# Performance work log

Hardware: AMD Instinct MI355X
Metric: run time of the kernel (lower is better)

The kernel has to match this reference:

```python
import jax, jax.numpy as jnp
import numpy as np

PI = np.pi
B_IN, B1, B2 = 30, 10, 6      # bandwidths: input S2, after conv1, after conv2
F1, F2, F_OUT = 20, 40, 10


def _wigner_d_stack(l, betas):
    """Wigner-d d^l_{mn}(beta) = <m|exp(-i beta Jy)|n> (real), shape [nbeta, 2l+1, 2l+1]."""
    n = 2 * l + 1
    m = np.arange(-l, l)
    c = np.sqrt(l * (l + 1) - m * (m + 1))          # J+ couplings m -> m+1
    Jp = np.zeros((n, n))
    Jp[np.arange(1, n), np.arange(n - 1)] = c
    A = 0.5 * (Jp.T - Jp)                            # exp(beta*A) = d^l(beta)
    ev, V = np.linalg.eig(A)
    Vi = np.linalg.inv(V)
    E = np.exp(np.multiply.outer(np.asarray(betas, np.float64), ev))
    return np.einsum('mk,bk,kn->bmn', V, E, Vi).real


def _qw(b):
    """Driscoll-Healy quadrature weights over beta for the SOFT grid of bandwidth b."""
    j = np.arange(2 * b)
    theta = PI * (2 * j + 1) / (4 * b)
    k = np.arange(b)
    return (2.0 / b) * np.sin(theta) * (np.sin(theta[:, None] * (2 * k + 1)) / (2 * k + 1)).sum(1)


def _betas(b):
    return PI * (2 * np.arange(2 * b) + 1) / (4 * b)


def _s2_grid():   # s2_near_identity_grid(): 3 betas x 8 alphas = 24 points
    beta = np.arange(1, 4) * (PI / 8) / 3
    alpha = np.linspace(0, 2 * PI, 8, endpoint=False)
    B, A = np.meshgrid(beta, alpha, indexing='ij')
    return B.ravel(), A.ravel()


def _so3_grid():  # so3_near_identity_grid(): 3x8x8 = 192 points, gamma = pre_gamma - alpha
    beta = np.arange(1, 4) * (PI / 8) / 3
    alpha = np.linspace(0, 2 * PI, 8, endpoint=False)
    pre_gamma = np.linspace(-2 * PI, 2 * PI, 8, endpoint=False)
    B, A, C = np.meshgrid(beta, alpha, pre_gamma, indexing='ij')
    return B.ravel(), A.ravel(), (C - A).ravel()


# ---------- static spectral constants (numpy, built once at import) ----------
_bet_in, _w_in = _betas(B_IN), _qw(B_IN)
_bet1, _w1 = _betas(B1), _qw(B1)
_bet2, _w2 = _betas(B2), _qw(B2)
_gb, _ga = _s2_grid()
_gb3, _ga3, _gc3 = _so3_grid()

# conv1 analysis: w(beta) * d^l_{m0}(beta_in), flattened over (l,m), l < B1
_dm1, _mi1, _y1 = [], [], []
for l in range(B1):
    d = _wigner_d_stack(l, _bet_in)                        # [60, 2l+1, 2l+1]
    _dm1.append((d[:, :, l] * _w_in[:, None]).T)           # [2l+1, 60] (column n=0)
    m = np.arange(-l, l + 1)
    _mi1.append(m % (2 * B_IN))
    dg = _wigner_d_stack(l, _gb)[:, :, l]                  # [24, 2l+1]
    _y1.append(np.exp(-1j * np.outer(m, _ga)) * dg.T)      # kernel rft basis [2l+1, 24]
DM1 = np.concatenate(_dm1, 0).astype(np.float32)           # [100, 60]
MI1 = np.concatenate(_mi1, 0)
Y1B = np.concatenate(_y1, 0).astype(np.complex64)          # [100, 24]

D_B1 = [_wigner_d_stack(l, _bet1) for l in range(B1)]      # d^l at the 20 betas of b=10 grid

# conv2 analysis: w(beta) * d^l_{mn}(beta_1), flattened over (l,m,n), l < B2
_dm2, _mi2, _ni2, _y2 = [], [], [], []
for l in range(B2):
    m = np.arange(-l, l + 1)
    d = D_B1[l]                                            # [20, 2l+1, 2l+1]
    _dm2.append((d * _w1[:, None, None]).reshape(2 * B1, -1).T)   # [(2l+1)^2, 20]
    mm, nn = np.meshgrid(m, m, indexing='ij')
    _mi2.append(mm.ravel() % (2 * B1))
    _ni2.append(nn.ravel() % (2 * B1))
    dg = _wigner_d_stack(l, _gb3)                          # [192, 2l+1, 2l+1]
    ph = np.exp(-1j * (np.multiply.outer(m, _ga3)[:, None, :] +
                       np.multiply.outer(m, _gc3)[None, :, :]))   # [2l+1,2l+1,192]
    _y2.append((np.moveaxis(dg, 0, -1) * ph).reshape(-1, _gb3.size))
DM2 = np.concatenate(_dm2, 0).astype(np.float32)           # [286, 20]
MI2 = np.concatenate(_mi2, 0)
NI2 = np.concatenate(_ni2, 0)
Y2B = np.concatenate(_y2, 0).astype(np.complex64)          # [286, 192]

D_B1F = [d.astype(np.float32) for d in D_B1]
D_B2F = [_wigner_d_stack(l, _bet2).astype(np.float32) for l in range(B2)]

SC1 = np.float32(1.0 / np.sqrt(_gb.size * 1))    # kernel scalings (s2cnn-style init scale)
SC2 = np.float32(1.0 / np.sqrt(_gb3.size * F1))
W2J = _w2.astype(np.float32)
INTEG_SCALE = np.float32((2 * PI / (2 * B2)) ** 2)


def _forward(x, kernel1, kernel2, w_out, bias_out):
    Bt = x.shape[0]
    # ---- S2Convolution: S2-FFT(x), rft(kernel), s2_mm, SO3-iFFT ----
    xh = jnp.fft.fft(x, axis=-1) / (2 * B_IN)                     # [B,1,60,60] cplx (alpha FFT)
    xg = xh[..., jnp.asarray(MI1)]                                # [B,1,60,100]
    X = jnp.einsum('kj,bfjk->kbf', jnp.asarray(DM1), xg)          # [100,B,1] spectral F^l_m
    Yk = jnp.einsum('kg,iog->kio', jnp.asarray(Y1B), kernel1.astype(jnp.complex64)) * SC1
    S = jnp.zeros((Bt, F1, 2 * B1, 2 * B1, 2 * B1), jnp.complex64)
    off = 0
    for l in range(B1):
        L = 2 * l + 1
        Z = jnp.einsum('mbi,nio->mnbo', X[off:off + L], jnp.conj(Yk[off:off + L]))
        T = jnp.einsum('jmn,mnbo->bojmn', float(2 * l + 1) * jnp.asarray(D_B1F[l]), Z)
        mi = np.arange(-l, l + 1) % (2 * B1)
        S = S.at[:, :, :, mi[:, None], mi[None, :]].add(T)
        off += L
    x1 = jnp.fft.ifft2(S, axes=(-2, -1)).real * float((2 * B1) ** 2)   # [B,F1,20,20,20]
    x1 = jax.nn.relu(x1)
    # ---- SO3Convolution: SO3-FFT, rft(kernel), so3_mm, SO3-iFFT ----
    xh2 = jnp.fft.fft2(x1, axes=(-2, -1)) / float((2 * B1) ** 2)       # alpha,gamma FFT
    xg2 = xh2[:, :, :, jnp.asarray(MI2), jnp.asarray(NI2)]             # [B,F1,20,286]
    X2 = jnp.einsum('kj,bfjk->kbf', jnp.asarray(DM2), xg2)             # [286,B,F1]
    Yk2 = jnp.einsum('kg,iog->kio', jnp.asarray(Y2B), kernel2.astype(jnp.complex64)) * SC2
    S2 = jnp.zeros((Bt, F2, 2 * B2, 2 * B2, 2 * B2), jnp.complex64)
    off = 0
    for l in range(B2):
        L = 2 * l + 1
        X2l = X2[off:off + L * L].reshape(L, L, Bt, F1)     # [m,k,B,i]
        Y2l = Yk2[off:off + L * L].reshape(L, L, F1, F2)    # [n,k,i,o]
        Z = jnp.einsum('mkbi,nkio->mnbo', X2l, jnp.conj(Y2l))   # hat z^l = hat x^l hat y^l+
        T = jnp.einsum('jmn,mnbo->bojmn', float(2 * l + 1) * jnp.asarray(D_B2F[l]), Z)
        mi = np.arange(-l, l + 1) % (2 * B2)
        S2 = S2.at[:, :, :, mi[:, None], mi[None, :]].add(T)
        off += L * L
    x2 = jnp.fft.ifft2(S2, axes=(-2, -1)).real * float((2 * B2) ** 2)  # [B,F2,12,12,12]
    x2 = jax.nn.relu(x2)
    # ---- so3_integrate + linear head ----
    feat = INTEG_SCALE * jnp.einsum('bfjac,j->bf', x2, jnp.asarray(W2J))
    return feat @ w_out.T + bias_out


def setup_inputs() -> dict:
    key = jax.random.key(0)
    ks = jax.random.split(key, 5)
    return {
        'x': jax.random.normal(ks[0], (128, 1, 2 * B_IN, 2 * B_IN), jnp.float32),
        'kernel1': jax.random.normal(ks[1], (1, F1, 24), jnp.float32),
        'kernel2': jax.random.normal(ks[2], (F1, F2, 192), jnp.float32),
        'w_out': jax.random.normal(ks[3], (F_OUT, F2), jnp.float32) / np.sqrt(float(F2)),
        'bias_out': jax.random.normal(ks[4], (F_OUT,), jnp.float32) * 0.01,
    }


def reference(x, kernel1, kernel2, w_out, bias_out):
    return _forward(x, kernel1, kernel2, w_out, bias_out)
```

## Files before the change

kernel.cpp:

```cpp
#include <hip/hip_runtime.h>
#include <cmath>

#define NT 256
#define BT 128

#define OFF_W60   0
#define OFF_E20   2280
#define OFF_E12   2320
#define OFF_W2J   2344
#define OFF_DM1   2356
#define OFF_Y1B   8356
#define OFF_D1R   13156
#define OFF_DM2   39756
#define OFF_Y2B   45476
#define OFF_D2R   155300
#define OFF_T19U  158732
#define OFF_T11V  159492
#define OFF_T12U  159932
#define OFF_TABA  160196
#define OFF_TABB  161526
#define OFF_TH19  161812
#define OFF_TH12  162212
#define OFF_TABH  162356
#define OFF_TAH1  162504
#define OFF_DM2T  163220
#define OFF_TGIX  168940
#define OFF_QW30  169228
#define OFF_QW10  169288
#define OFF_QW6   169308
#define OFF_D3B   169320
#define OFF_PA    170178
#define OFF_PG    170354
#define OFF_END   171764
#define N_INIT1   1742
#define N_INIT2   109735

__constant__ int c_ZB1[10] = {0,1,10,35,84,165,286,455,680,969};
__constant__ int c_ZBH[10] = {0,1,7,22,50,95,161,252,372,525};
__constant__ int c_ZB2[6]  = {0,1,10,35,84,165};
__constant__ int c_BOFF[6] = {0,22,208,718,1712,3350};

__device__ inline void wsync() {
    __asm__ volatile("" ::: "memory");
    __builtin_amdgcn_s_waitcnt(0xC07F);
    __builtin_amdgcn_wave_barrier();
    __asm__ volatile("" ::: "memory");
}

__device__ inline double dipow(double x, int e) {
    double r = 1.0;
    for (int i = 0; i < e; ++i) r *= x;
    return r;
}

__device__ double wigd(const double* F, const double* Fi, int l, int mp, int m, double beta) {
    double cb = cos(beta * 0.5), sb = sin(beta * 0.5);
    int smin = m - mp; if (smin < 0) smin = 0;
    int smax = l + m;  if (l - mp < smax) smax = l - mp;
    double pref = sqrt(F[l+mp] * F[l-mp] * F[l+m] * F[l-m]);
    double sum = 0.0;
    for (int s = smin; s <= smax; ++s) {
        double t = pref * (Fi[l+m-s] * Fi[s] * Fi[mp-m+s] * Fi[l-mp-s]);
        t *= dipow(cb, 2*l + m - mp - 2*s) * dipow(sb, mp - m + 2*s);
        sum += ((mp - m + s) & 1) ? -t : t;
    }
    return sum;
}

__device__ double qwj(int bnd, int j) {
    const double PI = 3.14159265358979323846;
    double theta = PI * (2*j + 1) / (4.0 * bnd);
    double s = 0.0;
    for (int k = 0; k < bnd; ++k) s += sin(theta * (2*k + 1)) / (2*k + 1);
    return 2.0 / bnd * sin(theta) * s;
}

__global__ void k_init1(float* __restrict__ ws) {
    int idx = blockIdx.x * blockDim.x + threadIdx.x;
    if (idx >= N_INIT1) return;
    double F[20], Fi[20];
    F[0] = 1.0;
    #pragma unroll
    for (int i = 1; i < 20; ++i) F[i] = F[i-1] * i;
    Fi[19] = 1.0 / F[19];
    #pragma unroll
    for (int i = 18; i >= 0; --i) Fi[i] = Fi[i+1] * (i+1);
    const double PI = 3.14159265358979323846;

    if (idx < 60) {
        ws[OFF_QW30 + idx] = (float)qwj(30, idx);
    } else if (idx < 80) {
        ws[OFF_QW10 + idx - 60] = (float)qwj(10, idx - 60);
    } else if (idx < 92) {
        ws[OFF_QW6 + idx - 80] = (float)qwj(6, idx - 80);
    } else if (idx < 950) {
        int e = idx - 92; int k2 = e / 3, bi = e % 3;
        int l = 0; while (l < 5 && k2 >= c_ZB2[l+1]) ++l;
        int L = 2*l + 1, loc = k2 - c_ZB2[l];
        int m = loc / L - l, n = loc % L - l;
        double beta = (bi + 1) * (PI / 8.0) / 3.0;
        ws[OFF_D3B + e] = (float)wigd(F, Fi, l, m, n, beta);
    } else if (idx < 1038) {
        int e = idx - 950; int m = e / 8 - 5, ai = e % 8;
        double ph = -(double)m * (2.0 * PI * ai / 8.0);
        ws[OFF_PA + 2*e]     = (float)cos(ph);
        ws[OFF_PA + 2*e + 1] = (float)sin(ph);
    } else {
        int e = idx - 1038; int n = e / 64 - 5, g2 = e % 64, ai = g2 / 8, ci = g2 % 8;
        double alpha = 2.0 * PI * ai / 8.0;
        double gamma = (-2.0 * PI + ci * (PI / 2.0)) - alpha;
        double ph = -(double)n * gamma;
        ws[OFF_PG + 2*e]     = (float)cos(ph);
        ws[OFF_PG + 2*e + 1] = (float)sin(ph);
    }
}

__global__ void k_init2(float* __restrict__ ws) {
    int idx = blockIdx.x * blockDim.x + threadIdx.x;
    if (idx >= N_INIT2) return;
    double F[20], Fi[20];
    F[0] = 1.0;
    #pragma unroll
    for (int i = 1; i < 20; ++i) F[i] = F[i-1] * i;
    Fi[19] = 1.0 / F[19];
    #pragma unroll
    for (int i = 18; i >= 0; --i) Fi[i] = Fi[i+1] * (i+1);
    const double PI = 3.14159265358979323846;

    if (idx < 1140) {
        int r = idx / 60, a = idx % 60;
        double ang = -2.0 * PI * (double)((r - 9) * a) / 60.0;
        ws[OFF_W60 + 2*idx]     = (float)cos(ang);
        ws[OFF_W60 + 2*idx + 1] = (float)sin(ang);
    } else if (idx < 1160) {
        int t = idx - 1140;
        double ang = 2.0 * PI * t / 20.0;
        ws[OFF_E20 + 2*t]     = (float)cos(ang);
        ws[OFF_E20 + 2*t + 1] = (float)sin(ang);
    } else if (idx < 1172) {
        int t = idx - 1160;
        double ang = 2.0 * PI * t / 12.0;
        ws[OFF_E12 + 2*t]     = (float)cos(ang);
        ws[OFF_E12 + 2*t + 1] = (float)sin(ang);
    } else if (idx < 1184) {
        int j = idx - 1172;
        ws[OFF_W2J + j] = ws[OFF_QW6 + j];
    } else if (idx < 7184) {
        int e = idx - 1184; int k = e / 60, j = e % 60;
        int l = 0; while ((l + 1) * (l + 1) <= k) ++l;
        int m = k - l*l - l;
        double beta = PI * (2*j + 1) / 120.0;
        ws[OFF_DM1 + e] = (float)((double)ws[OFF_QW30 + j] * wigd(F, Fi, l, m, 0, beta));
    } else if (idx < 9584) {
        int e = idx - 7184; int k = e / 24, g = e % 24;
        int l = 0; while ((l + 1) * (l + 1) <= k) ++l;
        int m = k - l*l - l;
        int bi = g / 8, ai = g % 8;
        double beta  = (bi + 1) * (PI / 8.0) / 3.0;
        double alpha = 2.0 * PI * ai / 8.0;
        double d = wigd(F, Fi, l, m, 0, beta);
        double ph = -(double)m * alpha;
        ws[OFF_Y1B + 2*e]     = (float)(d * cos(ph));
        ws[OFF_Y1B + 2*e + 1] = (float)(d * sin(ph));
    } else if (idx < 36184) {
        int e = idx - 9584; int j = e / 1330, t = e % 1330;
        int l = 0; while (l < 9 && t >= c_ZB1[l+1]) ++l;
        int L = 2*l + 1, loc = t - c_ZB1[l];
        int mi = loc / L, ni = loc % L;
        double beta = PI * (2*j + 1) / 40.0;
        ws[OFF_D1R + e] = (float)((double)L * wigd(F, Fi, l, mi - l, ni - l, beta));
    } else if (idx < 41904) {
    } else if (idx < 96816) {
        int e = idx - 41904; int k2 = e / 192, g = e % 192;
        int l = 0; while (l < 5 && k2 >= c_ZB2[l+1]) ++l;
        int L = 2*l + 1, loc = k2 - c_ZB2[l];
        int m = loc / L - l, n = loc % L - l;
        int bi = g / 64, ai = (g / 8) % 8, ci = g % 8;
        float d = ws[OFF_D3B + k2 * 3 + bi];
        const float2 pa = ((const float2*)(ws + OFF_PA))[(m + 5) * 8 + ai];
        const float2 pg = ((const float2*)(ws + OFF_PG))[(n + 5) * 64 + ai * 8 + ci];
        ws[OFF_Y2B + 2*e]     = d * (pa.x * pg.x - pa.y * pg.y);
        ws[OFF_Y2B + 2*e + 1] = d * (pa.x * pg.y + pa.y * pg.x);
    } else if (idx < 100248) {
        int e = idx - 96816; int j = e / 286, t = e % 286;
        int l = 0; while (l < 5 && t >= c_ZB2[l+1]) ++l;
        int L = 2*l + 1, loc = t - c_ZB2[l];
        int mi = loc / L, ni = loc % L;
        double beta = PI * (2*j + 1) / 24.0;
        ws[OFF_D2R + e] = (float)((double)L * wigd(F, Fi, l, mi - l, ni - l, beta));
    } else if (idx < 100628) {
        int e = idx - 100248; int c = e / 19, n = e % 19 - 9;
        double ang = 2.0 * PI * (double)(n * c) / 20.0;
        ws[OFF_T19U + 2*e]     = (float)cos(ang);
        ws[OFF_T19U + 2*e + 1] = (float)sin(ang);
    } else if (idx < 100848) {
        int e = idx - 100628; int r = e / 20, c = e % 20;
        double ang = -2.0 * PI * (double)((r - 5) * c) / 20.0;
        ws[OFF_T11V + 2*e]     = (float)cos(ang);
        ws[OFF_T11V + 2*e + 1] = (float)sin(ang);
    } else if (idx < 100980) {
        int e = idx - 100848; int c = e / 11, n = e % 11 - 5;
        double ang = 2.0 * PI * (double)(n * c) / 12.0;
        ws[OFF_T12U + 2*e]     = (float)cos(ang);
        ws[OFF_T12U + 2*e + 1] = (float)sin(ang);
    } else if (idx < 102310) {
    } else if (idx < 102596) {
        int t = idx - 102310;
        int l = 0; while (l < 5 && t >= c_ZB2[l+1]) ++l;
        int L = 2*l + 1, loc = t - c_ZB2[l];
        ((int*)ws)[OFF_TABB + t] = l | ((loc / L) << 8) | ((loc % L) << 16);
    } else if (idx < 102796) {
        int e = idx - 102596; int a = e / 10, mm = e % 10;
        double f = (mm == 0) ? 1.0 : 2.0;
        double ang = 2.0 * PI * (double)(mm * a) / 20.0;
        ws[OFF_TH19 + 2*e]     = (float)(f * cos(ang));
        ws[OFF_TH19 + 2*e + 1] = (float)(f * sin(ang));
    } else if (idx < 102868) {
        int e = idx - 102796; int a = e / 6, mm = e % 6;
        double f = (mm == 0) ? 1.0 : 2.0;
        double ang = 2.0 * PI * (double)(mm * a) / 12.0;
        ws[OFF_TH12 + 2*e]     = (float)(f * cos(ang));
        ws[OFF_TH12 + 2*e + 1] = (float)(f * sin(ang));
    } else if (idx < 103014) {
        int t = idx - 102868;
        int l = 0, cum = 0, loc = 0;
        for (; l < 6; ++l) {
            int L = 2*l + 1, h = (L*L + 1) / 2;
            if (t < cum + h) { loc = t - cum; break; }
            cum += h;
        }
        ((int*)ws)[OFF_TABH + t] = l | (loc << 8);
    } else if (idx < 103729) {
        int t = idx - 103014;
        int l = 0; while (l < 9 && t >= c_ZBH[l+1]) ++l;
        int L = 2*l + 1, loc = t - c_ZBH[l];
        ((int*)ws)[OFF_TAH1 + t] = l | ((loc / L) << 8) | ((loc % L) << 16);
    } else if (idx < 109449) {
        int e = idx - 103729; int k2 = e / 20, j = e % 20;
        int l = 0; while (l < 5 && k2 >= c_ZB2[l+1]) ++l;
        int L = 2*l + 1, loc = k2 - c_ZB2[l];
        int mi = loc / L, ni = loc % L;
        double beta = PI * (2*j + 1) / 40.0;
        ws[OFF_DM2T + e] = (float)((double)ws[OFF_QW10 + j] *
                                   wigd(F, Fi, l, mi - l, ni - l, beta) / 400.0);
    } else {
        int t = idx - 109449;
        int l = 0; while (l < 5 && t >= c_ZB2[l+1]) ++l;
        int L = 2*l + 1, loc = t - c_ZB2[l];
        int m = loc / L - l, n = loc % L - l;
        int gi, sgbit;
        if (m >= 0) { gi = m * 11 + (n + 5); sgbit = 0; }
        else        { gi = (-m) * 11 + (5 - n); sgbit = 1; }
        ((int*)ws)[OFF_TGIX + t] = gi | (sgbit << 16);
    }
}

__global__ void k_dft_alpha(const float* __restrict__ x, const float2* __restrict__ W60,
                            float2* __restrict__ xh) {
    int idx = blockIdx.x * blockDim.x + threadIdx.x;
    if (idx >= BT * 60 * 19) return;
    int r = idx % 19;
    int j = (idx / 19) % 60;
    int b = idx / (19 * 60);
    const float* xr = x + (b * 60 + j) * 60;
    const float2* wr = W60 + r * 60;
    float re = 0.f, im = 0.f;
    for (int a = 0; a < 60; ++a) {
        float v = xr[a];
        float2 w = wr[a];
        re += v * w.x; im += v * w.y;
    }
    xh[idx] = make_float2(re * (1.f / 60.f), im * (1.f / 60.f));
}

__global__ void k_X1Y1(const float2* __restrict__ xh, const float* __restrict__ DM1,
                       float2* __restrict__ X, const float* __restrict__ k1,
                       const float2* __restrict__ Y1B, float2* __restrict__ Yk1) {
    int bid = blockIdx.x;
    if (bid < 50) {
        int idx = bid * NT + threadIdx.x;
        if (idx >= 100 * BT) return;
        int b = idx % BT, k = idx / BT;
        int l = 0; while ((l + 1) * (l + 1) <= k) ++l;
        int r = (k - l*l - l) + 9;
        float re = 0.f, im = 0.f;
        for (int j = 0; j < 60; ++j) {
            float d = DM1[k * 60 + j];
            float2 v = xh[(b * 60 + j) * 19 + r];
            re += d * v.x; im += d * v.y;
        }
        X[k * BT + b] = make_float2(re, im);
    } else {
        int idx = (bid - 50) * NT + threadIdx.x;
        if (idx >= 100 * 20) return;
        int o = idx % 20, k = idx / 20;
        float re = 0.f, im = 0.f;
        for (int g = 0; g < 24; ++g) {
            float2 y = Y1B[k * 24 + g];
            float w = k1[o * 24 + g];
            re += y.x * w; im += y.y * w;
        }
        const float SC1 = 0.20412414523193154f;
        Yk1[idx] = make_float2(re * SC1, im * SC1);
    }
}

__global__ __launch_bounds__(NT) void k_Yk2(const float* __restrict__ k2in,
                                            const float2* __restrict__ Y2B,
                                            const int* __restrict__ gTABH,
                                            float2* __restrict__ Yk2) {
    const int h = blockIdx.x >> 1;
    const int half = blockIdx.x & 1;
    const int tid = threadIdx.x;
    int ph = gTABH[h];
    int l = ph & 255, loc = ph >> 8;
    int L = 2 * l + 1;
    int mi = loc / L, ni = loc % L;
    int k2  = c_ZB2[l] + loc;
    int locm = L * L - 1 - loc;
    int k2m = c_ZB2[l] + locm;
    float par = ((mi + ni) & 1) ? -1.f : 1.f;

    __shared__ __align__(16) float2 sY[192];
    for (int t = tid; t < 192; t += NT) sY[t] = Y2B[k2 * 192 + t];
    __syncthreads();
    const float4* sY4 = (const float4*)sY;
    const float SC2 = 0.016137430609197573f;
    for (int t = half * 400 + tid; t < half * 400 + 400; t += NT) {
        int o = t / 20, i = t % 20;
        const float4* kp = (const float4*)(k2in + (i * 40 + o) * 192);
        float re = 0.f, im = 0.f;
        #pragma unroll 4
        for (int p = 0; p < 48; ++p) {
            float4 w = kp[p];
            float4 y01 = sY4[2*p], y23 = sY4[2*p + 1];
            re += w.x * y01.x + w.y * y01.z + w.z * y23.x + w.w * y23.z;
            im += w.x * y01.y + w.y * y01.w + w.z * y23.y + w.w * y23.w;
        }
        re *= SC2; im *= SC2;
        Yk2[(o * 286 + k2) * 20 + i] = make_float2(re, im);
        if (k2m != k2)
            Yk2[(o * 286 + k2m) * 20 + i] = make_float2(par * re, -par * im);
    }
}

__global__ __launch_bounds__(NT) void k_stage1(
    const float2* __restrict__ X, const float2* __restrict__ Yk1,
    const float* __restrict__ gD1R,
    const float2* __restrict__ gT19, const float2* __restrict__ gT11,
    const float2* __restrict__ gTH19,
    const int* __restrict__ gTAH1, float2* __restrict__ Gg) {
    const int b = blockIdx.x % BT;
    const int f = blockIdx.x / BT;
    const int tid = threadIdx.x;
    const int wv = tid >> 6, lane = tid & 63;

    __shared__ __align__(16) float2 sZ[715];
    __shared__ __align__(16) float2 sT19[440];
    __shared__ __align__(16) float2 sTH19[280];
    __shared__ __align__(16) float2 sT11[220];
    __shared__ __align__(16) float2 sA[4][224];
    __shared__ __align__(16) float2 sB[4][280];

    for (int t = tid; t < 380; t += NT) sT19[(t / 19) * 22 + (t % 19)] = gT19[t];
    for (int t = tid; t < 200; t += NT) sTH19[(t / 10) * 14 + (t % 10)] = gTH19[t];
    for (int t = tid; t < 220; t += NT) sT11[t] = gT11[t];
    for (int t = tid; t < 715; t += NT) {
        int p = gTAH1[t];
        int l = p & 255, mm = (p >> 8) & 255, ni = p >> 16;
        float2 a = X[(l*l + l + mm) * BT + b];
        float2 y = Yk1[(l*l + ni) * 20 + f];
        sZ[t] = make_float2(a.x * y.x + a.y * y.y, a.y * y.x - a.x * y.y);
    }
    __syncthreads();

    float2* S   = sA[wv];
    float2* U   = sB[wv];
    float*  x1  = (float*)sA[wv];
    float2* V   = sB[wv];

    for (int jj = 0; jj < 5; ++jj) {
        const int j = wv + 4 * jj;

        {
            const float* dp = gD1R + j * 1330;
            for (int t = lane; t < 190; t += 64) {
                int mm = t / 19, ni = t % 19;
                int n = ni - 9;
                int an = n < 0 ? -n : n;
                int lmin = mm > an ? mm : an;
                float re = 0.f, im = 0.f;
                for (int l = lmin; l < 10; ++l) {
                    int L = 2*l + 1;
                    float dv = dp[c_ZB1[l] + (mm + l) * L + (n + l)];
                    float2 z = sZ[c_ZBH[l] + mm * L + (n + l)];
                    re += dv * z.x; im += dv * z.y;
                }
                S[mm * 22 + ni] = make_float2(re, im);
            }
        }
        wsync();

        for (int t = lane; t < 100; t += 64) {
            int mm = t / 10, c = t % 10;
            const float4* sp = (const float4*)(S + mm * 22);
            const float4* tp = (const float4*)(sT19 + c * 22);
            float re_e = 0.f, im_e = 0.f, re_o = 0.f, im_o = 0.f;
            #pragma unroll
            for (int p = 0; p < 9; ++p) {
                float4 s = sp[p], w = tp[p];
                re_o += s.x * w.x - s.y * w.y;  im_o += s.x * w.y + s.y * w.x;
                re_e += s.z * w.z - s.w * w.w;  im_e += s.z * w.w + s.w * w.z;
            }
            {
                float2 s1 = S[mm * 22 + 18], w1 = sT19[c * 22 + 18];
                re_o += s1.x * w1.x - s1.y * w1.y;
                im_o += s1.x * w1.y + s1.y * w1.x;
            }
            U[c * 14 + mm]        = make_float2(re_e + re_o, im_e + im_o);
            U[(c + 10) * 14 + mm] = make_float2(re_e - re_o, im_e - im_o);
        }
        wsync();

        for (int t = lane; t < 100; t += 64) {
            int cp = t % 10, ap = t / 10;
            const float4* u0 = (const float4*)(U + cp * 14);
            const float4* u1 = (const float4*)(U + (cp + 10) * 14);
            const float4* tp = (const float4*)(sTH19 + ap * 14);
            float e0 = 0.f, o0 = 0.f, e1 = 0.f, o1 = 0.f;
            #pragma unroll
            for (int p = 0; p < 5; ++p) {
                float4 w = tp[p];
                float4 ua = u0[p], ub = u1[p];
                e0 += ua.x * w.x - ua.y * w.y;
                o0 += ua.z * w.z - ua.w * w.w;
                e1 += ub.x * w.x - ub.y * w.y;
                o1 += ub.z * w.z - ub.w * w.w;
            }
            float v;
            v = e0 + o0; x1[ap * 20 + cp]             = v > 0.f ? v : 0.f;
            v = e0 - o0; x1[(ap + 10) * 20 + cp]      = v > 0.f ? v : 0.f;
            v = e1 + o1; x1[ap * 20 + cp + 10]        = v > 0.f ? v : 0.f;
            v = e1 - o1; x1[(ap + 10) * 20 + cp + 10] = v > 0.f ? v : 0.f;
        }
        wsync();

        for (int t = lane; t < 120; t += 64) {
            int nn = t / 20, a = t % 20;
            const float4* xp = (const float4*)(x1 + a * 20);
            const float4* tp = (const float4*)(sT11 + (nn + 5) * 20);
            float r0 = 0.f, i0 = 0.f, r1 = 0.f, i1 = 0.f;
            #pragma unroll
            for (int p = 0; p < 5; ++p) {
                float4 xv = xp[p];
                float4 t01 = tp[2*p], t23 = tp[2*p + 1];
                r0 += xv.x * t01.x + xv.y * t01.z;
                i0 += xv.x * t01.y + xv.y * t01.w;
                r1 += xv.z * t23.x + xv.w * t23.z;
                i1 += xv.z * t23.y + xv.w * t23.w;
            }
            V[nn * 22 + a] = make_float2(r0 + r1, i0 + i1);
        }
        wsync();

        for (int t = lane; t < 66; t += 64) {
            int mm = t / 11, ni2 = t % 11;
            int nn2 = ni2 - 5;
            int na = nn2 < 0 ? -nn2 : nn2;
            float s = nn2 < 0 ? -1.f : 1.f;
            const float4* vp = (const float4*)(V + na * 22);
            const float4* tp = (const float4*)(sT11 + (mm + 5) * 20);
            float r0 = 0.f, i0 = 0.f, r1 = 0.f, i1 = 0.f;
            #pragma unroll
            for (int q = 0; q < 10; ++q) {
                float4 v = vp[q], w = tp[q];
                float vy0 = s * v.y, vy1 = s * v.w;
                r0 += v.x * w.x - vy0 * w.y;
                i0 += v.x * w.y + vy0 * w.x;
                r1 += v.z * w.z - vy1 * w.w;
                i1 += v.z * w.w + vy1 * w.z;
            }
            Gg[((size_t)(b * 20 + f) * 20 + j) * 66 + t] = make_float2(r0 + r1, i0 + i1);
        }
        wsync();
    }
}

__global__ __launch_bounds__(NT) void k_X2c(
    const float2* __restrict__ Gg, const float* __restrict__ gDM2T,
    const int* __restrict__ gTGIX, float2* __restrict__ X2g) {
    const int b = blockIdx.x % BT;
    const int f = blockIdx.x / BT;
    const int tid = threadIdx.x;
    __shared__ __align__(16) float2 sG[1320];
    const float2* Gp = Gg + (size_t)(b * 20 + f) * 20 * 66;
    for (int t = tid; t < 1320; t += NT) sG[t] = Gp[t];
    __syncthreads();
    for (int k2 = tid; k2 < 286; k2 += NT) {
        int e = gTGIX[k2];
        int gi = e & 0xFFFF;
        float sg = (e >> 16) ? -1.f : 1.f;
        const float* dm = gDM2T + k2 * 20;
        float re = 0.f, im = 0.f;
        #pragma unroll
        for (int j = 0; j < 20; ++j) {
            float d = dm[j];
            float2 g = sG[j * 66 + gi];
            re += d * g.x; im += d * g.y;
        }
        X2g[b * 5720 + k2 * 20 + f] = make_float2(re, sg * im);
    }
}

__global__ __launch_bounds__(NT) void k_Z2(
    const float2* __restrict__ X2g, const float2* __restrict__ Yk2,
    const int* __restrict__ gTABB, const int* __restrict__ gTABH,
    float2* __restrict__ Z2g) {
    const int bt   = blockIdx.x & 15;
    const int part = (blockIdx.x >> 4) & 1;
    const int o    = blockIdx.x >> 5;
    const int b0 = bt * 8;
    const int tid = threadIdx.x;

    __shared__ __align__(16) float2 sB[3350];

    const int sub  = part ? 3350 : 0;
    const int stN  = part ? 2420 : 3300;
    const int k2b  = part ? 165 : 0;
    const float2* Bg = Yk2 + o * 5720 + k2b * 20;
    for (int e = tid; e < stN; e += NT) {
        int k2 = k2b + e / 20, i = e % 20;
        int p = gTABB[k2];
        int l = p & 255, r = (p >> 8) & 255, kk = p >> 16;
        sB[c_BOFF[l] - sub + r * (40 * l + 22) + kk * 20 + i] = Bg[e];
    }
    __syncthreads();

    const int perb  = part ? 61 : 85;
    const int hbase = part ? 85 : 0;
    for (int q = tid; q < 8 * perb; q += NT) {
        int b_local = q / perb, h = hbase + q % perb;
        int ph = gTABH[h];
        int l = ph & 255, loc = ph >> 8;
        int L = 2 * l + 1;
        int mi = loc / L, ni = loc % L;
        const float4* ap = (const float4*)(X2g + (size_t)(b0 + b_local) * 5720
                                           + (c_ZB2[l] + mi * L) * 20);
        const float4* bp = (const float4*)(sB + c_BOFF[l] - sub + ni * (40 * l + 22));
        float re = 0.f, im = 0.f;
        int n4 = 10 * L;
        for (int p4 = 0; p4 < n4; ++p4) {
            float4 a = ap[p4], y = bp[p4];
            re += a.x * y.x + a.y * y.y + a.z * y.z + a.w * y.w;
            im += a.y * y.x - a.x * y.y + a.w * y.z - a.z * y.w;
        }
        size_t base = ((size_t)(b0 + b_local) * 40 + o) * 286;
        Z2g[base + c_ZB2[l] + loc] = make_float2(re, im);
        int locm = L * L - 1 - loc;
        if (locm != loc) {
            float sg = ((mi + ni) & 1) ? -1.f : 1.f;
            Z2g[base + c_ZB2[l] + locm] = make_float2(sg * re, -sg * im);
        }
    }
}

__global__ __launch_bounds__(NT) void k_stage2b(
    const float2* __restrict__ Z2g, const float* __restrict__ gD2R,
    const float2* __restrict__ gT12, const float2* __restrict__ gTH12,
    const float* __restrict__ gW2J, float* __restrict__ feat) {
    const int b = blockIdx.x % BT;
    const int o = blockIdx.x / BT;
    const int tid = threadIdx.x;
    const int wv = tid >> 6, lane = tid & 63;

    __shared__ __align__(16) float2 sZb[286];
    __shared__ __align__(16) float2 sT12[168];
    __shared__ __align__(16) float2 sTH12[96];
    __shared__ __align__(16) float2 sS[4][88];
    __shared__ __align__(16) float2 sU[4][96];
    __shared__ float sredw[4];

    const float2* Zr = Z2g + ((size_t)b * 40 + o) * 286;
    for (int t = tid; t < 286; t += NT) sZb[t] = Zr[t];
    for (int t = tid; t < 132; t += NT) sT12[(t / 11) * 14 + (t % 11)] = gT12[t];
    for (int t = tid; t < 72; t += NT) sTH12[(t / 6) * 8 + (t % 6)] = gTH12[t];
    __syncthreads();

    float2* S = sS[wv];
    float2* U = sU[wv];
    float facc = 0.f;

    for (int jj = 0; jj < 3; ++jj) {
        const int j = wv + 4 * jj;

        {
            const float* dp = gD2R + j * 286;
            for (int t = lane; t < 66; t += 64) {
                int mm = t / 11, ni = t % 11;
                int n = ni - 5;
                int an = n < 0 ? -n : n;
                int lmin = mm > an ? mm : an;
                float re = 0.f, im = 0.f;
                for (int l = lmin; l < 6; ++l) {
                    int L = 2*l + 1;
                    int off = c_ZB2[l] + (mm + l) * L + (n + l);
                    float dv = dp[off];
                    float2 z = sZb[off];
                    re += dv * z.x; im += dv * z.y;
                }
                S[mm * 14 + ni] = make_float2(re, im);
            }
        }
        wsync();

        for (int t = lane; t < 72; t += 64) {
            int mm = t / 12, c = t % 12;
            const float4* sp = (const float4*)(S + mm * 14);
            const float4* tp = (const float4*)(sT12 + c * 14);
            float re = 0.f, im = 0.f;
            #pragma unroll
            for (int p = 0; p < 5; ++p) {
                float4 s = sp[p], w = tp[p];
                re += s.x * w.x - s.y * w.y + s.z * w.z - s.w * w.w;
                im += s.x * w.y + s.y * w.x + s.z * w.w + s.w * w.z;
            }
            float2 s1 = S[mm * 14 + 10], w1 = sT12[c * 14 + 10];
            re += s1.x * w1.x - s1.y * w1.y;
            im += s1.x * w1.y + s1.y * w1.x;
            U[c * 8 + mm] = make_float2(re, im);
        }
        wsync();

        {
            float wj = gW2J[j];
            for (int t = lane; t < 144; t += 64) {
                int a = t / 12, c = t % 12;
                const float4* up = (const float4*)(U + c * 8);
                const float4* tp = (const float4*)(sTH12 + a * 8);
                float acc = 0.f;
                #pragma unroll
                for (int p = 0; p < 3; ++p) {
                    float4 u = up[p], w = tp[p];
                    acc += u.x * w.x - u.y * w.y + u.z * w.z - u.w * w.w;
                }
                if (acc > 0.f) facc += wj * acc;
            }
        }
        wsync();
    }

    #pragma unroll
    for (int d = 32; d > 0; d >>= 1) facc += __shfl_down(facc, d, 64);
    if (lane == 0) sredw[wv] = facc;
    __syncthreads();
    if (tid == 0) {
        const float INTEG = 0.27415567780803774f;
        feat[b * 40 + o] = (sredw[0] + sredw[1] + sredw[2] + sredw[3]) * INTEG;
    }
}

__global__ void k_out(const float* __restrict__ feat, const float* __restrict__ w,
                      const float* __restrict__ bias, float* __restrict__ out) {
    int idx = blockIdx.x * blockDim.x + threadIdx.x;
    if (idx >= BT * 10) return;
    int fo = idx % 10, b = idx / 10;
    float acc = bias[fo];
    for (int o2 = 0; o2 < 40; ++o2) acc += feat[b * 40 + o2] * w[fo * 40 + o2];
    out[idx] = acc;
}

extern "C" void kernel_launch(void* const* d_in, const int* in_sizes, int n_in,
                              void* d_out, int out_size, void* d_ws, size_t ws_size,
                              hipStream_t stream) {
    (void)in_sizes; (void)n_in; (void)out_size; (void)ws_size;
    const float* x   = (const float*)d_in[0];
    const float* k1  = (const float*)d_in[1];
    const float* k2  = (const float*)d_in[2];
    const float* wO  = (const float*)d_in[3];
    const float* bO  = (const float*)d_in[4];
    float* out = (float*)d_out;

    float* ws = (float*)d_ws;
    const float2* cW60 = (const float2*)(ws + OFF_W60);
    const float*  cW2J = ws + OFF_W2J;
    const float*  cDM1 = ws + OFF_DM1;
    const float2* cY1B = (const float2*)(ws + OFF_Y1B);
    const float*  gD1R = ws + OFF_D1R;
    const float2* cY2B = (const float2*)(ws + OFF_Y2B);
    const float*  gD2R = ws + OFF_D2R;
    const float2* gT19 = (const float2*)(ws + OFF_T19U);
    const float2* gT11 = (const float2*)(ws + OFF_T11V);
    const float2* gT12 = (const float2*)(ws + OFF_T12U);
    const float2* gTH19 = (const float2*)(ws + OFF_TH19);
    const float2* gTH12 = (const float2*)(ws + OFF_TH12);
    const int*    gTABB = (const int*)(ws + OFF_TABB);
    const int*    gTABH = (const int*)(ws + OFF_TABH);
    const int*    gTAH1 = (const int*)(ws + OFF_TAH1);
    const float*  gDM2T = ws + OFF_DM2T;
    const int*    gTGIX = (const int*)(ws + OFF_TGIX);

    float2* xh   = (float2*)(ws + OFF_END);
    float2* X    = xh + BT * 60 * 19;
    float2* Yk1  = X + 100 * BT;
    float2* Yk2  = Yk1 + 100 * 20;
    float2* X2   = Yk2 + 40 * 286 * 20;
    float*  feat = (float*)(X2 + (size_t)BT * 5720);
    float2* Gg   = (float2*)(feat + BT * 40);
    float2* Z2   = Gg;

    k_init1<<<(N_INIT1 + NT - 1) / NT, NT, 0, stream>>>(ws);
    k_init2<<<(N_INIT2 + NT - 1) / NT, NT, 0, stream>>>(ws);
    k_dft_alpha<<<(BT * 60 * 19 + NT - 1) / NT, NT, 0, stream>>>(x, cW60, xh);
    k_X1Y1<<<58, NT, 0, stream>>>(xh, cDM1, X, k1, cY1B, Yk1);
    k_Yk2<<<292, NT, 0, stream>>>(k2, cY2B, gTABH, Yk2);
    k_stage1<<<BT * 20, NT, 0, stream>>>(X, Yk1, gD1R, gT19, gT11, gTH19, gTAH1, Gg);
    k_X2c<<<BT * 20, NT, 0, stream>>>(Gg, gDM2T, gTGIX, X2);
    k_Z2<<<1280, NT, 0, stream>>>(X2, Yk2, gTABB, gTABH, Z2);
    k_stage2b<<<BT * 40, NT, 0, stream>>>(Z2, gD2R, gT12, gTH12, cW2J, feat);
    k_out<<<(BT * 10 + NT - 1) / NT, NT, 0, stream>>>(feat, wO, bO, out);
}
```

Measured before the change: 397.5 us.

## Fuse alpha DFT with conv1 analysis and fold X2 contraction into stage1

```diff
diff --git a/kernel.cpp b/kernel.cpp
--- a/kernel.cpp
+++ b/kernel.cpp
@@ -255,43 +255,48 @@
     }
 }
 
-__global__ void k_dft_alpha(const float* __restrict__ x, const float2* __restrict__ W60,
-                            float2* __restrict__ xh) {
-    int idx = blockIdx.x * blockDim.x + threadIdx.x;
-    if (idx >= BT * 60 * 19) return;
-    int r = idx % 19;
-    int j = (idx / 19) % 60;
-    int b = idx / (19 * 60);
-    const float* xr = x + (b * 60 + j) * 60;
-    const float2* wr = W60 + r * 60;
-    float re = 0.f, im = 0.f;
-    for (int a = 0; a < 60; ++a) {
-        float v = xr[a];
-        float2 w = wr[a];
-        re += v * w.x; im += v * w.y;
-    }
-    xh[idx] = make_float2(re * (1.f / 60.f), im * (1.f / 60.f));
-}
-
-__global__ void k_X1Y1(const float2* __restrict__ xh, const float* __restrict__ DM1,
-                       float2* __restrict__ X, const float* __restrict__ k1,
-                       const float2* __restrict__ Y1B, float2* __restrict__ Yk1) {
-    int bid = blockIdx.x;
-    if (bid < 50) {
-        int idx = bid * NT + threadIdx.x;
-        if (idx >= 100 * BT) return;
-        int b = idx % BT, k = idx / BT;
-        int l = 0; while ((l + 1) * (l + 1) <= k) ++l;
-        int r = (k - l*l - l) + 9;
-        float re = 0.f, im = 0.f;
-        for (int j = 0; j < 60; ++j) {
-            float d = DM1[k * 60 + j];
-            float2 v = xh[(b * 60 + j) * 19 + r];
-            re += d * v.x; im += d * v.y;
-        }
-        X[k * BT + b] = make_float2(re, im);
+__global__ __launch_bounds__(NT) void k_front(
+    const float* __restrict__ x, const float2* __restrict__ W60,
+    const float* __restrict__ DM1, float2* __restrict__ X,
+    const float* __restrict__ k1, const float2* __restrict__ Y1B,
+    float2* __restrict__ Yk1) {
+    const int bid = blockIdx.x;
+    const int tid = threadIdx.x;
+    if (bid < BT) {
+        const int b = bid;
+        __shared__ __align__(16) float  sx[3600];
+        __shared__ __align__(16) float2 sW[1140];
+        __shared__ __align__(16) float2 sxh[1140];
+        for (int t = tid; t < 900; t += NT)
+            ((float4*)sx)[t] = ((const float4*)(x + b * 3600))[t];
+        for (int t = tid; t < 1140; t += NT) sW[t] = W60[t];
+        __syncthreads();
+        for (int t = tid; t < 1140; t += NT) {
+            int r = t % 19, j = t / 19;
+            const float* xr = sx + j * 60;
+            const float2* wr = sW + r * 60;
+            float re = 0.f, im = 0.f;
+            for (int a = 0; a < 60; ++a) {
+                float v = xr[a];
+                float2 w = wr[a];
+                re += v * w.x; im += v * w.y;
+            }
+            sxh[j * 19 + r] = make_float2(re * (1.f / 60.f), im * (1.f / 60.f));
+        }
+        __syncthreads();
+        for (int k = tid; k < 100; k += NT) {
+            int l = 0; while ((l + 1) * (l + 1) <= k) ++l;
+            int r = (k - l*l - l) + 9;
+            float re = 0.f, im = 0.f;
+            for (int j = 0; j < 60; ++j) {
+                float d = DM1[k * 60 + j];
+                float2 v = sxh[j * 19 + r];
+                re += d * v.x; im += d * v.y;
+            }
+            X[k * BT + b] = make_float2(re, im);
+        }
     } else {
-        int idx = (bid - 50) * NT + threadIdx.x;
+        int idx = (bid - BT) * NT + tid;
         if (idx >= 100 * 20) return;
         int o = idx % 20, k = idx / 20;
         float re = 0.f, im = 0.f;
@@ -349,7 +354,8 @@
     const float* __restrict__ gD1R,
     const float2* __restrict__ gT19, const float2* __restrict__ gT11,
     const float2* __restrict__ gTH19,
-    const int* __restrict__ gTAH1, float2* __restrict__ Gg) {
+    const int* __restrict__ gTAH1, const float* __restrict__ gDM2T,
+    const int* __restrict__ gTGIX, float2* __restrict__ X2g) {
     const int b = blockIdx.x % BT;
     const int f = blockIdx.x / BT;
     const int tid = threadIdx.x;
@@ -359,6 +365,7 @@
     __shared__ __align__(16) float2 sT19[440];
     __shared__ __align__(16) float2 sTH19[280];
     __shared__ __align__(16) float2 sT11[220];
+    __shared__ __align__(16) float2 sGall[1320];
     __shared__ __align__(16) float2 sA[4][224];
     __shared__ __align__(16) float2 sB[4][280];
 
@@ -480,22 +487,12 @@
                 r1 += v.z * w.z - vy1 * w.w;
                 i1 += v.z * w.w + vy1 * w.z;
             }
-            Gg[((size_t)(b * 20 + f) * 20 + j) * 66 + t] = make_float2(r0 + r1, i0 + i1);
+            sGall[j * 66 + t] = make_float2(r0 + r1, i0 + i1);
         }
         wsync();
     }
-}
-
-__global__ __launch_bounds__(NT) void k_X2c(
-    const float2* __restrict__ Gg, const float* __restrict__ gDM2T,
-    const int* __restrict__ gTGIX, float2* __restrict__ X2g) {
-    const int b = blockIdx.x % BT;
-    const int f = blockIdx.x / BT;
-    const int tid = threadIdx.x;
-    __shared__ __align__(16) float2 sG[1320];
-    const float2* Gp = Gg + (size_t)(b * 20 + f) * 20 * 66;
-    for (int t = tid; t < 1320; t += NT) sG[t] = Gp[t];
     __syncthreads();
+
     for (int k2 = tid; k2 < 286; k2 += NT) {
         int e = gTGIX[k2];
         int gi = e & 0xFFFF;
@@ -505,7 +502,7 @@
         #pragma unroll
         for (int j = 0; j < 20; ++j) {
             float d = dm[j];
-            float2 g = sG[j * 66 + gi];
+            float2 g = sGall[j * 66 + gi];
             re += d * g.x; im += d * g.y;
         }
         X2g[b * 5720 + k2 * 20 + f] = make_float2(re, sg * im);
@@ -564,7 +561,7 @@
     }
 }
 
-__global__ __launch_bounds__(NT) void k_stage2b(
+__global__ __launch_bounds__(128) void k_stage2b(
     const float2* __restrict__ Z2g, const float* __restrict__ gD2R,
     const float2* __restrict__ gT12, const float2* __restrict__ gTH12,
     const float* __restrict__ gW2J, float* __restrict__ feat) {
@@ -576,22 +573,22 @@
     __shared__ __align__(16) float2 sZb[286];
     __shared__ __align__(16) float2 sT12[168];
     __shared__ __align__(16) float2 sTH12[96];
-    __shared__ __align__(16) float2 sS[4][88];
-    __shared__ __align__(16) float2 sU[4][96];
-    __shared__ float sredw[4];
+    __shared__ __align__(16) float2 sS[2][88];
+    __shared__ __align__(16) float2 sU[2][96];
+    __shared__ float sredw[2];
 
     const float2* Zr = Z2g + ((size_t)b * 40 + o) * 286;
-    for (int t = tid; t < 286; t += NT) sZb[t] = Zr[t];
-    for (int t = tid; t < 132; t += NT) sT12[(t / 11) * 14 + (t % 11)] = gT12[t];
-    for (int t = tid; t < 72; t += NT) sTH12[(t / 6) * 8 + (t % 6)] = gTH12[t];
+    for (int t = tid; t < 286; t += 128) sZb[t] = Zr[t];
+    for (int t = tid; t < 132; t += 128) sT12[(t / 11) * 14 + (t % 11)] = gT12[t];
+    for (int t = tid; t < 72; t += 128) sTH12[(t / 6) * 8 + (t % 6)] = gTH12[t];
     __syncthreads();
 
     float2* S = sS[wv];
     float2* U = sU[wv];
     float facc = 0.f;
 
-    for (int jj = 0; jj < 3; ++jj) {
-        const int j = wv + 4 * jj;
+    for (int jj = 0; jj < 6; ++jj) {
+        const int j = wv + 2 * jj;
 
         {
             const float* dp = gD2R + j * 286;
@@ -655,7 +652,7 @@
     __syncthreads();
     if (tid == 0) {
         const float INTEG = 0.27415567780803774f;
-        feat[b * 40 + o] = (sredw[0] + sredw[1] + sredw[2] + sredw[3]) * INTEG;
+        feat[b * 40 + o] = (sredw[0] + sredw[1]) * INTEG;
     }
 }
 
@@ -699,23 +696,20 @@
     const float*  gDM2T = ws + OFF_DM2T;
     const int*    gTGIX = (const int*)(ws + OFF_TGIX);
 
-    float2* xh   = (float2*)(ws + OFF_END);
-    float2* X    = xh + BT * 60 * 19;
+    float2* X    = (float2*)(ws + OFF_END);
     float2* Yk1  = X + 100 * BT;
     float2* Yk2  = Yk1 + 100 * 20;
     float2* X2   = Yk2 + 40 * 286 * 20;
     float*  feat = (float*)(X2 + (size_t)BT * 5720);
-    float2* Gg   = (float2*)(feat + BT * 40);
-    float2* Z2   = Gg;
+    float2* Z2   = (float2*)(feat + BT * 40);
 
     k_init1<<<(N_INIT1 + NT - 1) / NT, NT, 0, stream>>>(ws);
     k_init2<<<(N_INIT2 + NT - 1) / NT, NT, 0, stream>>>(ws);
-    k_dft_alpha<<<(BT * 60 * 19 + NT - 1) / NT, NT, 0, stream>>>(x, cW60, xh);
-    k_X1Y1<<<58, NT, 0, stream>>>(xh, cDM1, X, k1, cY1B, Yk1);
+    k_front<<<BT + 8, NT, 0, stream>>>(x, cW60, cDM1, X, k1, cY1B, Yk1);
     k_Yk2<<<292, NT, 0, stream>>>(k2, cY2B, gTABH, Yk2);
-    k_stage1<<<BT * 20, NT, 0, stream>>>(X, Yk1, gD1R, gT19, gT11, gTH19, gTAH1, Gg);
-    k_X2c<<<BT * 20, NT, 0, stream>>>(Gg, gDM2T, gTGIX, X2);
+    k_stage1<<<BT * 20, NT, 0, stream>>>(X, Yk1, gD1R, gT19, gT11, gTH19, gTAH1,
+                                         gDM2T, gTGIX, X2);
     k_Z2<<<1280, NT, 0, stream>>>(X2, Yk2, gTABB, gTABH, Z2);
-    k_stage2b<<<BT * 40, NT, 0, stream>>>(Z2, gD2R, gT12, gTH12, cW2J, feat);
+    k_stage2b<<<BT * 40, 128, 0, stream>>>(Z2, gD2R, gT12, gTH12, cW2J, feat);
     k_out<<<(BT * 10 + NT - 1) / NT, NT, 0, stream>>>(feat, wO, bO, out);
 }
```

New measurement: 363.6 us (median of 2 runs). -8.5%, faster.
